# Performance work log

Hardware: AMD Instinct MI355X
Metric: run time of the kernel (lower is better)

The kernel has to match this reference:

```python
import jax, jax.numpy as jnp
import numpy as np
from jax import lax

EPS = 1e-5

@jax.custom_vjp
def bin_active(x):
    # forward: sign binarization (original also returns channel-mean of |x|, which is discarded)
    return jnp.sign(x)

def _ba_fwd(x):
    return jnp.sign(x), x

def _ba_bwd(x, g):
    # straight-through estimator: zero grad where |x| >= 1
    return (jnp.where((x >= 1.0) | (x <= -1.0), 0.0, g),)

bin_active.defvjp(_ba_fwd, _ba_bwd)


def setup_inputs() -> dict:
    key = jax.random.key(0)
    k1, k2 = jax.random.split(key)
    N, C_in, H, W_sp = 64, 256, 56, 56
    C_out, K = 256, 3
    x = jax.random.normal(k1, (N, C_in, H, W_sp), dtype=jnp.float32)
    gamma = jnp.ones((C_in,), dtype=jnp.float32)
    beta = jnp.zeros((C_in,), dtype=jnp.float32)
    W = jax.random.normal(k2, (C_out, C_in, K, K), dtype=jnp.float32) * 0.05
    return {"x": x, "gamma": gamma, "beta": beta, "W": W}


def reference(x, gamma, beta, W):
    # BatchNorm2d (training-mode batch stats), affine
    mean = jnp.mean(x, axis=(0, 2, 3), keepdims=True)          # [1,C,1,1]
    var = jnp.var(x, axis=(0, 2, 3), keepdims=True)
    xn = (x - mean) * lax.rsqrt(var + EPS)
    xn = xn * gamma.reshape(1, -1, 1, 1) + beta.reshape(1, -1, 1, 1)
    # binarize activations
    xb = bin_active(xn)
    # Conv2d stride=1 pad=1, no bias, then ReLU
    y = lax.conv_general_dilated(
        xb, W,
        window_strides=(1, 1),
        padding=[(1, 1), (1, 1)],
        dimension_numbers=("NCHW", "OIHW", "NCHW"),
    )
    return jax.nn.relu(y)
```

## Files before the change

### kernel.cpp

```cpp
#include <hip/hip_runtime.h>
#include <hip/hip_bf16.h>
#include <stdint.h>

#define HP 58
#define CIN 256
#define COUT 256
#define HH 56
#define WW 56
#define XROW 14848
#define SROW 928
#define IMG_STRIDE (HP*XROW)
#define NPIX 200704.0

#define XO    16
#define AO    89600
#define LDS_TOTAL 155136

typedef __attribute__((ext_vector_type(4)))  int i32x4;
typedef __attribute__((ext_vector_type(16))) int i32x16;

#define GLDS(g, l) __builtin_amdgcn_global_load_lds( \
    (const __attribute__((address_space(1))) void*)(g), \
    (__attribute__((address_space(3))) void*)(l), 16, 0, 0)

__global__ __launch_bounds__(256) void prep_a(const float* __restrict__ x,
                                              double* __restrict__ part,
                                              const float* __restrict__ W,
                                              int8_t* __restrict__ Wbr,
                                              float* __restrict__ invs) {
  if (blockIdx.x < 16384) {
    int b = blockIdx.x;
    int c = b >> 6, n = b & 63;
    const float4* p = (const float4*)(x + (size_t)(n*CIN + c) * (HH*WW));
    double s = 0.0, s2 = 0.0;
    for (int i = threadIdx.x; i < 784; i += 256) {
      float4 v = p[i];
      double a0 = v.x, a1 = v.y, a2 = v.z, a3 = v.w;
      s  += (a0 + a1) + (a2 + a3);
      s2 += (a0*a0 + a1*a1) + (a2*a2 + a3*a3);
    }
    for (int off = 32; off > 0; off >>= 1) {
      s  += __shfl_down(s, off);
      s2 += __shfl_down(s2, off);
    }
    __shared__ double red[8];
    int wv = threadIdx.x >> 6, ln = threadIdx.x & 63;
    if (ln == 0) { red[wv*2] = s; red[wv*2+1] = s2; }
    __syncthreads();
    if (threadIdx.x == 0) {
      double ts = ((red[0]+red[2])+red[4])+red[6];
      double t2 = ((red[1]+red[3])+red[5])+red[7];
      part[(size_t)(c*64 + n)*2]     = ts;
      part[(size_t)(c*64 + n)*2 + 1] = t2;
    }
  } else {
    int co = blockIdx.x - 16384, ci = threadIdx.x;
    float w[9]; float mx = 0.f;
    const float* p = W + (size_t)co*(CIN*9) + ci*9;
    #pragma unroll
    for (int t = 0; t < 9; ++t) { w[t] = p[t]; mx = fmaxf(mx, fabsf(w[t])); }
    for (int off = 32; off > 0; off >>= 1) mx = fmaxf(mx, __shfl_xor(mx, off));
    __shared__ float sm[4];
    if ((threadIdx.x & 63) == 0) sm[threadIdx.x >> 6] = mx;
    __syncthreads();
    mx = fmaxf(fmaxf(sm[0], sm[1]), fmaxf(sm[2], sm[3]));
    float s = mx > 0.f ? 127.f / mx : 0.f;
    int off = ((ci >> 6) * 4 + ((ci >> 4) & 3)) * 4096 + co*16 + (ci & 15);
    #pragma unroll
    for (int t = 0; t < 9; ++t) {
      int qv = (int)lrintf(w[t] * s);
      qv = qv > 127 ? 127 : (qv < -127 ? -127 : qv);
      Wbr[t*65536 + off] = (int8_t)qv;
    }
    if (threadIdx.x == 0) invs[co] = mx / 127.f;
  }
}

__global__ __launch_bounds__(64) void stats_final(const double* __restrict__ part,
                                                  const float* __restrict__ gamma,
                                                  const float* __restrict__ beta,
                                                  double* __restrict__ prm) {
  int c = blockIdx.x, ln = threadIdx.x;
  double s  = part[(size_t)(c*64 + ln)*2];
  double s2 = part[(size_t)(c*64 + ln)*2 + 1];
  for (int off = 32; off > 0; off >>= 1) {
    s  += __shfl_down(s, off);
    s2 += __shfl_down(s2, off);
  }
  if (ln == 0) {
    double mean = s / NPIX;
    double var  = s2 / NPIX - mean*mean;
    double inv  = 1.0 / sqrt(var + 1e-5);
    prm[c*4+0] = mean;
    prm[c*4+1] = (double)gamma[c] * inv;
    prm[c*4+2] = (double)beta[c];
  }
}

__global__ __launch_bounds__(256) void binarize(const float* __restrict__ x,
                                                const double* __restrict__ prm,
                                                int8_t* __restrict__ xb) {
  int b = blockIdx.x;
  int n = b / HP, y = b % HP;
  int8_t* orow = xb + (size_t)(n*HP + y) * XROW;
  if (y == 0 || y == HP-1) {
    int4 z = {0,0,0,0};
    int4* q = (int4*)orow;
    for (int i = threadIdx.x; i < XROW/16; i += 256) q[i] = z;
    return;
  }
  __shared__ char sbuf[WW][260];
  int h  = y - 1;
  int tid = threadIdx.x;
  #pragma unroll
  for (int it = 0; it < 14; ++it) {
    int t = it*256 + tid;
    int c = t / 14, j = t - c*14;
    float4 v = *(const float4*)(x + (size_t)(n*CIN + c)*(HH*WW) + h*WW + j*4);
    double mu = prm[c*4], gi = prm[c*4+1], be = prm[c*4+2];
    #pragma unroll
    for (int e = 0; e < 4; ++e) {
      double xv = (double)((&v.x)[e]);
      double vv = (xv - mu)*gi + be;
      sbuf[j*4+e][c] = vv > 0.0 ? (int8_t)1 : (vv < 0.0 ? (int8_t)-1 : (int8_t)0);
    }
  }
  __syncthreads();
  for (int u = tid; u < 16*58; u += 256) {
    int slot = u / 58, xx = u - slot*58;
    int4 v = {0,0,0,0};
    if (xx >= 1 && xx <= WW) {
      const uint32_t* src = (const uint32_t*)&sbuf[xx-1][slot*16];
      v.x = src[0]; v.y = src[1]; v.z = src[2]; v.w = src[3];
    }
    *(int4*)(orow + u*16) = v;
  }
}

__global__ __launch_bounds__(512, 2) void conv_gemm(const int8_t* __restrict__ xb,
                                                    const int8_t* __restrict__ Wbr,
                                                    const float* __restrict__ invs,
                                                    float* __restrict__ out) {
  extern __shared__ char smem[];
  int bid = blockIdx.x;
  int swz = (bid & 7) * 112 + (bid >> 3);
  int n_img = swz / 14, rg = swz - n_img * 14;
  int y0 = 1 + rg * 4;

  int tid = threadIdx.x;
  int ln = tid & 63, wid = tid >> 6;
  int wm = wid >> 2, wn = wid & 3;

  size_t xoff = (size_t)n_img * IMG_STRIDE + (size_t)(y0 - 1) * XROW;

  #pragma unroll
  for (int i = 0; i < 11; ++i) {
    int o = tid*16 + i*8192;
    if (o < 6*XROW)
      GLDS(xb + xoff + o, smem + XO + o);
  }

  const int8_t* stSrc = Wbr + tid*16;
  char*         stDst = smem + AO + tid*16;
#define STAGE(SCOFF, BUFQ) do { \
    const int8_t* _s = stSrc + (SCOFF); \
    char* _d = stDst + (BUFQ)*16384; \
    GLDS(_s, _d); GLDS(_s + 8192, _d + 8192); \
  } while (0)

  i32x16 acc[4][2] = {};
  STAGE(0, 0); STAGE(16384, 1); STAGE(32768, 2);

  const char* vA = smem + AO + ((ln >> 5) << 12) + (wm*128 + (ln & 31)) * 16;
  const char* vX = smem + XO + wn*XROW + (ln >> 5)*SROW + ((ln & 31) - 1) * 16;

  i32x4 aA[4][2], bA[2][2], aB[4][2], bB[2][2];

#define LOADF(Q, SU, AV, BV) do { \
    const char* _ab = vA + (Q)*16384; \
    AV[0][0] = *(const i32x4*)(_ab +    0); AV[0][1] = *(const i32x4*)(_ab + 8192); \
    AV[1][0] = *(const i32x4*)(_ab +  512); AV[1][1] = *(const i32x4*)(_ab + 8704); \
    AV[2][0] = *(const i32x4*)(_ab + 1024); AV[2][1] = *(const i32x4*)(_ab + 9216); \
    AV[3][0] = *(const i32x4*)(_ab + 1536); AV[3][1] = *(const i32x4*)(_ab + 9728); \
    const char* _bb = vX + (SU); \
    BV[0][0] = *(const i32x4*)(_bb +    0); BV[0][1] = *(const i32x4*)(_bb + 1856); \
    BV[1][0] = *(const i32x4*)(_bb +  512); BV[1][1] = *(const i32x4*)(_bb + 2368); \
  } while (0)

#define MFMA_ALL(AV, BV) do { \
    __builtin_amdgcn_s_setprio(1); \
    _Pragma("unroll") \
    for (int ks = 0; ks < 2; ++ks) \
      _Pragma("unroll") \
      for (int mt = 0; mt < 4; ++mt) \
        _Pragma("unroll") \
        for (int nt = 0; nt < 2; ++nt) \
          acc[mt][nt] = __builtin_amdgcn_mfma_i32_32x32x32_i8(AV[mt][ks], BV[nt][ks], \
                                                              acc[mt][nt], 0, 0, 0); \
    __builtin_amdgcn_s_setprio(0); \
  } while (0)

#define VMB do { \
    asm volatile("s_waitcnt vmcnt(2)" ::: "memory"); \
    __builtin_amdgcn_s_barrier(); \
  } while (0)

  asm volatile("s_waitcnt vmcnt(4)" ::: "memory");
  __builtin_amdgcn_s_barrier();
  LOADF(0, 0, aA, bA);

  #pragma unroll 1
  for (int t = 0; t < 9; ++t) {
    int kh0 = (t * 11) >> 5,  kw0 = t - kh0*3;
    int t1  = t < 8 ? t + 1 : 8;
    int kh1 = (t1 * 11) >> 5, kw1 = t1 - kh1*3;
    int su0 = kh0*XROW + kw0*16;
    int su1 = su0 + 3712, su2 = su0 + 7424, su3 = su0 + 11136;
    int su4 = kh1*XROW + kw1*16;
    int sA  = 4*t;
    int sc3 = (sA+3 < 36 ? sA+3 : 35) * 16384;
    int sc4 = (sA+4 < 36 ? sA+4 : 35) * 16384;
    int sc5 = (sA+5 < 36 ? sA+5 : 35) * 16384;
    int sc6 = (sA+6 < 36 ? sA+6 : 35) * 16384;

    VMB; STAGE(sc3, 3); LOADF(1, su1, aB, bB); MFMA_ALL(aA, bA);
    VMB; STAGE(sc4, 0); LOADF(2, su2, aA, bA); MFMA_ALL(aB, bB);
    VMB; STAGE(sc5, 1); LOADF(3, su3, aB, bB); MFMA_ALL(aA, bA);
    VMB; STAGE(sc6, 2); LOADF(0, su4, aA, bA); MFMA_ALL(aB, bB);
  }
  asm volatile("s_waitcnt vmcnt(0)" ::: "memory");

  int y_out = y0 + wn - 1;
  size_t ob0 = ((size_t)n_img * COUT) * (HH*WW) + (size_t)y_out * WW;
  #pragma unroll
  for (int mt = 0; mt < 4; ++mt) {
    int cb0 = wm*128 + mt*32 + ((ln >> 5) << 2);
    float4 iv[4];
    #pragma unroll
    for (int q = 0; q < 4; ++q) iv[q] = *(const float4*)(invs + cb0 + 8*q);
    #pragma unroll
    for (int nt = 0; nt < 2; ++nt) {
      int xx = nt*32 + (ln & 31);
      bool ok = (xx >= 1) && (xx <= WW);
      size_t ob = ob0 + (xx - 1);
      #pragma unroll
      for (int r = 0; r < 16; ++r) {
        int q = r >> 2, rr = r & 3;
        int co = cb0 + 8*q + rr;
        float v = fmaxf((float)acc[mt][nt][r] * ((&iv[q].x)[rr]), 0.0f);
        if (ok) out[ob + (size_t)co * (HH*WW)] = v;
      }
    }
  }
}

extern "C" void kernel_launch(void* const* d_in, const int* in_sizes, int n_in,
                              void* d_out, int out_size, void* d_ws, size_t ws_size,
                              hipStream_t stream) {
  const float* x     = (const float*)d_in[0];
  const float* gamma = (const float*)d_in[1];
  const float* beta  = (const float*)d_in[2];
  const float* W     = (const float*)d_in[3];
  float* out = (float*)d_out;

  char* ws = (char*)d_ws;
  double*  part = (double*)ws;
  double*  prm  = (double*)(ws + 262144);
  float*   invs = (float*)(ws + 270336);
  int8_t*  Wbr  = (int8_t*)(ws + 271360);
  int8_t*  xbuf = (int8_t*)(ws + 1048576);

  (void)hipFuncSetAttribute((const void*)conv_gemm,
                            hipFuncAttributeMaxDynamicSharedMemorySize, LDS_TOTAL);

  hipLaunchKernelGGL(prep_a,      dim3(16640), dim3(256), 0, stream, x, part, W, Wbr, invs);
  hipLaunchKernelGGL(stats_final, dim3(256),   dim3(64),  0, stream, part, gamma, beta, prm);
  hipLaunchKernelGGL(binarize,    dim3(64*HP), dim3(256), 0, stream, x, prm, xbuf);
  hipLaunchKernelGGL(conv_gemm,   dim3(896),   dim3(512), LDS_TOTAL, stream, xbuf, Wbr, invs, out);
}
```

Before: 266.3 us.

## Make conv GEMM persistent with 256 blocks looping over row tiles

The conv GEMM grid drops from 896 one-shot blocks to 256 persistent blocks. Each block walks 3 or 4 contiguous (image, row-group) tiles, 896 tiles in total. While the epilogue stores the current tile's outputs, the next tile's input rows and first weight stages are prefetched, so prologue load latency hides behind output writes. This removes tail-wave imbalance (896 blocks over 256 CUs) but leaves uneven per-block work of 3 versus 4 tiles. It also adds a vmcnt(0) drain and a barrier between tiles.

```diff
diff --git a/kernel.cpp b/kernel.cpp
--- a/kernel.cpp
+++ b/kernel.cpp
@@ -143,22 +143,13 @@
                                                     float* __restrict__ out) {
   extern __shared__ char smem[];
   int bid = blockIdx.x;
-  int swz = (bid & 7) * 112 + (bid >> 3);
-  int n_img = swz / 14, rg = swz - n_img * 14;
-  int y0 = 1 + rg * 4;
+  int swz = (bid & 7) * 32 + (bid >> 3);
+  int T0 = (swz * 7) >> 1;
+  int T1 = ((swz + 1) * 7) >> 1;
 
   int tid = threadIdx.x;
   int ln = tid & 63, wid = tid >> 6;
   int wm = wid >> 2, wn = wid & 3;
-
-  size_t xoff = (size_t)n_img * IMG_STRIDE + (size_t)(y0 - 1) * XROW;
-
-  #pragma unroll
-  for (int i = 0; i < 11; ++i) {
-    int o = tid*16 + i*8192;
-    if (o < 6*XROW)
-      GLDS(xb + xoff + o, smem + XO + o);
-  }
 
   const int8_t* stSrc = Wbr + tid*16;
   char*         stDst = smem + AO + tid*16;
@@ -168,13 +159,19 @@
     GLDS(_s, _d); GLDS(_s + 8192, _d + 8192); \
   } while (0)
 
-  i32x16 acc[4][2] = {};
-  STAGE(0, 0); STAGE(16384, 1); STAGE(32768, 2);
+#define STAGE_X(XOFF) do { \
+    _Pragma("unroll") \
+    for (int _i = 0; _i < 11; ++_i) { \
+      int _o = tid*16 + _i*8192; \
+      if (_o < 6*XROW) GLDS(xb + (XOFF) + _o, smem + XO + _o); \
+    } \
+  } while (0)
 
   const char* vA = smem + AO + ((ln >> 5) << 12) + (wm*128 + (ln & 31)) * 16;
   const char* vX = smem + XO + wn*XROW + (ln >> 5)*SROW + ((ln & 31) - 1) * 16;
 
   i32x4 aA[4][2], bA[2][2], aB[4][2], bB[2][2];
+  i32x16 acc[4][2];
 
 #define LOADF(Q, SU, AV, BV) do { \
     const char* _ab = vA + (Q)*16384; \
@@ -205,53 +202,82 @@
     __builtin_amdgcn_s_barrier(); \
   } while (0)
 
+  {
+    int img0 = T0 / 14, rg0 = T0 - img0*14;
+    size_t xoff0 = (size_t)img0 * IMG_STRIDE + (size_t)(rg0*4) * XROW;
+    STAGE_X(xoff0);
+    STAGE(0, 0); STAGE(16384, 1); STAGE(32768, 2);
+  }
   asm volatile("s_waitcnt vmcnt(4)" ::: "memory");
   __builtin_amdgcn_s_barrier();
-  LOADF(0, 0, aA, bA);
 
   #pragma unroll 1
-  for (int t = 0; t < 9; ++t) {
-    int kh0 = (t * 11) >> 5,  kw0 = t - kh0*3;
-    int t1  = t < 8 ? t + 1 : 8;
-    int kh1 = (t1 * 11) >> 5, kw1 = t1 - kh1*3;
-    int su0 = kh0*XROW + kw0*16;
-    int su1 = su0 + 3712, su2 = su0 + 7424, su3 = su0 + 11136;
-    int su4 = kh1*XROW + kw1*16;
-    int sA  = 4*t;
-    int sc3 = (sA+3 < 36 ? sA+3 : 35) * 16384;
-    int sc4 = (sA+4 < 36 ? sA+4 : 35) * 16384;
-    int sc5 = (sA+5 < 36 ? sA+5 : 35) * 16384;
-    int sc6 = (sA+6 < 36 ? sA+6 : 35) * 16384;
-
-    VMB; STAGE(sc3, 3); LOADF(1, su1, aB, bB); MFMA_ALL(aA, bA);
-    VMB; STAGE(sc4, 0); LOADF(2, su2, aA, bA); MFMA_ALL(aB, bB);
-    VMB; STAGE(sc5, 1); LOADF(3, su3, aB, bB); MFMA_ALL(aA, bA);
-    VMB; STAGE(sc6, 2); LOADF(0, su4, aA, bA); MFMA_ALL(aB, bB);
+  for (int T = T0; T < T1; ++T) {
+    int img = T / 14, rg = T - img*14;
+    int y0 = 1 + rg*4;
+
+    #pragma unroll
+    for (int mt = 0; mt < 4; ++mt)
+      #pragma unroll
+      for (int nt = 0; nt < 2; ++nt)
+        acc[mt][nt] = (i32x16){};
+
+    LOADF(0, 0, aA, bA);
+
+    #pragma unroll 1
+    for (int t = 0; t < 9; ++t) {
+      int kh0 = (t * 11) >> 5,  kw0 = t - kh0*3;
+      int t1  = t < 8 ? t + 1 : 8;
+      int kh1 = (t1 * 11) >> 5, kw1 = t1 - kh1*3;
+      int su0 = kh0*XROW + kw0*16;
+      int su1 = su0 + 3712, su2 = su0 + 7424, su3 = su0 + 11136;
+      int su4 = kh1*XROW + kw1*16;
+      int sA  = 4*t;
+
+      VMB; if (sA+3 < 36) STAGE((sA+3)*16384, 3); LOADF(1, su1, aB, bB); MFMA_ALL(aA, bA);
+      VMB; if (sA+4 < 36) STAGE((sA+4)*16384, 0); LOADF(2, su2, aA, bA); MFMA_ALL(aB, bB);
+      VMB; if (sA+5 < 36) STAGE((sA+5)*16384, 1); LOADF(3, su3, aB, bB); MFMA_ALL(aA, bA);
+      VMB; if (sA+6 < 36) STAGE((sA+6)*16384, 2); LOADF(0, su4, aA, bA); MFMA_ALL(aB, bB);
+    }
+
+    __builtin_amdgcn_s_barrier();
+    if (T + 1 < T1) {
+      int Tn = T + 1;
+      int imgn = Tn / 14, rgn = Tn - imgn*14;
+      size_t xoffn = (size_t)imgn * IMG_STRIDE + (size_t)(rgn*4) * XROW;
+      STAGE_X(xoffn);
+      STAGE(0, 0); STAGE(16384, 1); STAGE(32768, 2);
+    }
+
+    int y_out = y0 + wn - 1;
+    size_t ob0 = ((size_t)img * COUT) * (HH*WW) + (size_t)y_out * WW;
+    #pragma unroll
+    for (int mt = 0; mt < 4; ++mt) {
+      int cb0 = wm*128 + mt*32 + ((ln >> 5) << 2);
+      float4 iv[4];
+      #pragma unroll
+      for (int q = 0; q < 4; ++q) iv[q] = *(const float4*)(invs + cb0 + 8*q);
+      #pragma unroll
+      for (int nt = 0; nt < 2; ++nt) {
+        int xx = nt*32 + (ln & 31);
+        bool ok = (xx >= 1) && (xx <= WW);
+        size_t ob = ob0 + (xx - 1);
+        #pragma unroll
+        for (int r = 0; r < 16; ++r) {
+          int q = r >> 2, rr = r & 3;
+          int co = cb0 + 8*q + rr;
+          float v = fmaxf((float)acc[mt][nt][r] * ((&iv[q].x)[rr]), 0.0f);
+          if (ok) out[ob + (size_t)co * (HH*WW)] = v;
+        }
+      }
+    }
+
+    if (T + 1 < T1) {
+      asm volatile("s_waitcnt vmcnt(0)" ::: "memory");
+      __builtin_amdgcn_s_barrier();
+    }
   }
   asm volatile("s_waitcnt vmcnt(0)" ::: "memory");
-
-  int y_out = y0 + wn - 1;
-  size_t ob0 = ((size_t)n_img * COUT) * (HH*WW) + (size_t)y_out * WW;
-  #pragma unroll
-  for (int mt = 0; mt < 4; ++mt) {
-    int cb0 = wm*128 + mt*32 + ((ln >> 5) << 2);
-    float4 iv[4];
-    #pragma unroll
-    for (int q = 0; q < 4; ++q) iv[q] = *(const float4*)(invs + cb0 + 8*q);
-    #pragma unroll
-    for (int nt = 0; nt < 2; ++nt) {
-      int xx = nt*32 + (ln & 31);
-      bool ok = (xx >= 1) && (xx <= WW);
-      size_t ob = ob0 + (xx - 1);
-      #pragma unroll
-      for (int r = 0; r < 16; ++r) {
-        int q = r >> 2, rr = r & 3;
-        int co = cb0 + 8*q + rr;
-        float v = fmaxf((float)acc[mt][nt][r] * ((&iv[q].x)[rr]), 0.0f);
-        if (ok) out[ob + (size_t)co * (HH*WW)] = v;
-      }
-    }
-  }
 }
 
 extern "C" void kernel_launch(void* const* d_in, const int* in_sizes, int n_in,
@@ -276,5 +302,5 @@
   hipLaunchKernelGGL(prep_a,      dim3(16640), dim3(256), 0, stream, x, part, W, Wbr, invs);
   hipLaunchKernelGGL(stats_final, dim3(256),   dim3(64),  0, stream, part, gamma, beta, prm);
   hipLaunchKernelGGL(binarize,    dim3(64*HP), dim3(256), 0, stream, x, prm, xbuf);
-  hipLaunchKernelGGL(conv_gemm,   dim3(896),   dim3(512), LDS_TOTAL, stream, xbuf, Wbr, invs, out);
-}
+  hipLaunchKernelGGL(conv_gemm,   dim3(256),   dim3(512), LDS_TOTAL, stream, xbuf, Wbr, invs, out);
+}
```

Result: slower. 279.4 us (+4.9%).
